# Optimization experiments

Hardware: AMD Instinct MI355X
Metric: run time of the kernel (lower is better)

The kernel has to match this reference:

```python
import jax, jax.numpy as jnp
import numpy as np

B, N, K = 8, 2048, 100  # graphs per batch, nodes per graph, diffpool clusters


def _bn(x, g, b, eps=1e-5):
    # BatchNorm1d in training mode over all B*N nodes (biased variance)
    m = x.mean(axis=(0, 1))
    v = x.var(axis=(0, 1))
    return (x - m) * jax.lax.rsqrt(v + eps) * g + b


def _norm_adj(A):
    # PyG gcn_norm: add remaining self-loops (fill=1), D^-1/2 (A+I) D^-1/2
    n = A.shape[-1]
    d = jnp.diagonal(A, axis1=-2, axis2=-1)
    A_hat = A + jnp.where(d == 0, 1.0, 0.0)[..., :, None] * jnp.eye(n, dtype=A.dtype)
    deg = A_hat.sum(-1)
    dinv = jnp.where(deg > 0, 1.0 / jnp.sqrt(deg), 0.0)
    return dinv[..., :, None] * A_hat * dinv[..., None, :]


def _gcn(An, x, W, b):
    # GCNConv: propagate(x @ W) + bias, with pre-normalized adjacency
    return An @ (x @ W) + b


def _forward(x, adj, W_in, W3030, Wp13, b30, b100, Wfc_pool, bfc_pool,
             W1, b1, W2, b2, gamma30, beta30, gamma100, beta100):
    A_w = _norm_adj(adj)                               # weighted (edge_attr) adjacency
    A_b = _norm_adj((adj > 0).astype(adj.dtype))       # pool convs ignore edge_attr
    # feature branch
    x11 = _bn(_gcn(A_w, x, W_in[0], b30[0]), gamma30[0], beta30[0])
    x12 = _bn(_gcn(A_w, x11, W3030[0], b30[1]), gamma30[1], beta30[1])
    x13 = _bn(_gcn(A_w, x12, W3030[1], b30[2]), gamma30[2], beta30[2])
    x1_out = jnp.concatenate([x11, x12, x13], -1).max(axis=1)   # [B,90]
    # assignment branch
    s11 = _bn(_gcn(A_b, x, W_in[1], b30[3]), gamma30[3], beta30[3])
    s12 = _bn(_gcn(A_b, s11, W3030[2], b30[4]), gamma30[4], beta30[4])
    s13 = _bn(_gcn(A_b, s12, Wp13, b100), gamma100, beta100)
    s1 = jnp.concatenate([s11, s12, s13], -1) @ Wfc_pool + bfc_pool  # [B,N,K]
    # dense_diff_pool (link/entropy losses are unused by the forward output)
    s = jax.nn.softmax(s1, -1)
    p1_x = jnp.einsum('bnk,bnd->bkd', s, x13)          # s^T x  [B,K,30]
    p1_adj = jnp.einsum('bnk,bnl->bkl', s, adj @ s)    # s^T A s  [B,K,K]
    # second stage on pooled (dense, weighted) graph
    A2 = _norm_adj(p1_adj)
    x21 = _bn(_gcn(A2, p1_x, W3030[3], b30[5]), gamma30[5], beta30[5])
    x22 = _bn(_gcn(A2, x21, W3030[4], b30[6]), gamma30[6], beta30[6])
    x23 = _bn(_gcn(A2, x22, W3030[5], b30[7]), gamma30[7], beta30[7])
    x2_out = jnp.concatenate([x21, x22, x23], -1).max(axis=1)   # [B,90]
    h = jnp.concatenate([x1_out, x2_out], -1) @ W1 + b1
    return jax.nn.relu(h) @ W2 + b2                    # [B,6]


def setup_inputs():
    key = jax.random.key(0)
    ks = jax.random.split(key, 12)
    u = jax.random.uniform(ks[0], (B, N, N), dtype=jnp.float32)
    mask = jax.random.uniform(ks[1], (B, N, N)) < 0.05
    A = jnp.triu(u * mask, 1)
    adj = A + jnp.swapaxes(A, -1, -2)
    x = jax.random.normal(ks[2], (B, N, 3), dtype=jnp.float32)
    w = lambda k, s: jax.random.normal(k, s, dtype=jnp.float32) * 0.1
    return dict(
        x=x, adj=adj,
        W_in=w(ks[3], (2, 3, 30)),      # conv11, pool_conv11
        W3030=w(ks[4], (6, 30, 30)),    # conv12, conv13, pool_conv12, conv21..23
        Wp13=w(ks[5], (30, 100)),
        b30=jnp.zeros((8, 30), jnp.float32),
        b100=jnp.zeros((100,), jnp.float32),
        Wfc_pool=w(ks[6], (160, 100)), bfc_pool=jnp.zeros((100,), jnp.float32),
        W1=w(ks[7], (180, 50)), b1=jnp.zeros((50,), jnp.float32),
        W2=w(ks[8], (50, 6)), b2=jnp.zeros((6,), jnp.float32),
        gamma30=jnp.ones((8, 30), jnp.float32), beta30=jnp.zeros((8, 30), jnp.float32),
        gamma100=jnp.ones((100,), jnp.float32), beta100=jnp.zeros((100,), jnp.float32),
    )


def reference(x, adj, W_in, W3030, Wp13, b30, b100, Wfc_pool, bfc_pool,
              W1, b1, W2, b2, gamma30, beta30, gamma100, beta100):
    return _forward(x, adj, W_in, W3030, Wp13, b30, b100, Wfc_pool, bfc_pool,
                    W1, b1, W2, b2, gamma30, beta30, gamma100, beta100)
```

## Files before the change

kernel.cpp:

```cpp
#include <hip/hip_runtime.h>
#include <hip/hip_fp16.h>
#include <cstdint>
#include <cstddef>

#define BATCH 8
#define NN 2048
#define RTOT 16384
#define CAP 176

static constexpr size_t OF_B1W   = 0;
static constexpr size_t OF_B1B   = 3840;
static constexpr size_t OF_B2W   = 7680;
static constexpr size_t OF_B2B   = 11520;
static constexpr size_t OF_B3W   = 15360;
static constexpr size_t OF_B3B   = 15840;
static constexpr size_t OF_S2    = 17440;
static constexpr size_t OF_CNT   = 17620;
static constexpr size_t ZEND     = 17632;
static constexpr size_t OF_ELLV  = 17664;
static constexpr size_t OF_ELLC  = OF_ELLV + 2883584;
static constexpr size_t OF_ROWLEN= OF_ELLC + 1441792;
static constexpr size_t OF_DINVW = OF_ROWLEN + 16384;
static constexpr size_t OF_DINVB = OF_DINVW + 16384;
static constexpr size_t OF_HWB   = OF_DINVB + 16384;
static constexpr size_t OF_HW3   = OF_HWB + 524288;
static constexpr size_t OF_HB100 = OF_HW3 + 262144;
static constexpr size_t OF_ZW    = OF_HB100 + 851968;
static constexpr size_t OF_ZB    = OF_ZW + 524288;
static constexpr size_t OF_X11   = OF_ZB + 1703936;
static constexpr size_t OF_X12   = OF_X11 + 524288;
static constexpr size_t OF_X13   = OF_X12 + 524288;
static constexpr size_t OF_S11   = OF_X13 + 524288;
static constexpr size_t OF_S12   = OF_S11 + 524288;
static constexpr size_t OF_PARTMAX = OF_S12 + 524288;
static constexpr size_t OF_PP    = OF_PARTMAX + 23040;
static constexpr size_t OF_PPOOL = OF_PP + 3328000;

#define FMA4(acc, s, h) { acc.x += (s)*(h).x; acc.y += (s)*(h).y; acc.z += (s)*(h).z; acc.w += (s)*(h).w; }

__device__ __forceinline__ unsigned short f2h(float f) {
  _Float16 h = (_Float16)f;
  return *(unsigned short*)&h;
}
__device__ __forceinline__ float h2f(unsigned short s) {
  _Float16 h = *(_Float16*)&s;
  return (float)h;
}
__device__ __forceinline__ float2 h2f2(unsigned int u) {
  __half2 h = *(__half2*)&u;
  return __half22float2(h);
}

struct __align__(8) us4 { unsigned short x, y, z, w; };

#define ACC8(g, wt) { \
  float2 f0=h2f2((g).x), f1=h2f2((g).y), f2=h2f2((g).z), f3=h2f2((g).w); \
  acc[0] += (wt)*f0.x; acc[1] += (wt)*f0.y; acc[2] += (wt)*f1.x; acc[3] += (wt)*f1.y; \
  acc[4] += (wt)*f2.x; acc[5] += (wt)*f2.y; acc[6] += (wt)*f3.x; acc[7] += (wt)*f3.y; }


__global__ __launch_bounds__(256) void k_build_ell(
    const float* __restrict__ adj, const float* __restrict__ x,
    const float* __restrict__ Win, float* __restrict__ ellv,
    unsigned short* __restrict__ ellc, int* __restrict__ rowlen,
    float* __restrict__ dinvw, float* __restrict__ dinvb,
    unsigned short* __restrict__ Hwb, float* __restrict__ zbase)
{
  int r = blockIdx.x;
  int t = threadIdx.x, lane = t & 63, wv = t >> 6;
  if (blockIdx.x < 69) {
    int zi = blockIdx.x * 256 + t;
    if (zi < (int)ZEND) zbase[zi] = 0.f;
  }
  const float* row = adj + (size_t)r * NN;
  __shared__ int wcnt[4];
  __shared__ float wsumA[4];
  __shared__ float dsh[2];
  float4 a = ((const float4*)row)[t];
  float4 b = ((const float4*)row)[256 + t];
  float vals[8] = {a.x, a.y, a.z, a.w, b.x, b.y, b.z, b.w};
  int cbase0 = t*4, cbase1 = 1024 + t*4;
  int cnt = 0; float sum = 0.f;
#pragma unroll
  for (int k = 0; k < 8; ++k) { sum += vals[k]; cnt += (vals[k] != 0.f) ? 1 : 0; }
  int pre = cnt;
#pragma unroll
  for (int o = 1; o < 64; o <<= 1) { int n = __shfl_up(pre, o); if (lane >= o) pre += n; }
  int excl = pre - cnt;
  int wtot = __shfl(pre, 63);
#pragma unroll
  for (int o = 32; o; o >>= 1) sum += __shfl_down(sum, o);
  if (lane == 0) { wcnt[wv] = wtot; wsumA[wv] = sum; }
  __syncthreads();
  int base = 0;
  for (int w = 0; w < wv; ++w) base += wcnt[w];
  int p = base + excl;
  size_t rb = (size_t)r * CAP;
#pragma unroll
  for (int k = 0; k < 8; ++k) {
    float v = vals[k];
    if (v != 0.f && p < CAP) {
      ellv[rb + p] = v;
      ellc[rb + p] = (unsigned short)((k < 4) ? (cbase0 + k) : (cbase1 + (k - 4)));
      ++p;
    }
  }
  if (t == 0) {
    int tot = wcnt[0] + wcnt[1] + wcnt[2] + wcnt[3];
    float ws = wsumA[0] + wsumA[1] + wsumA[2] + wsumA[3];
    int nnz = tot < CAP ? tot : CAP;
    int n = nnz;
    while ((n & 3) && n < CAP) { ellv[rb + n] = 0.f; ellc[rb + n] = 0; ++n; }
    rowlen[r] = n;
    float dw = rsqrtf(ws + 1.f), db = rsqrtf((float)nnz + 1.f);
    dinvw[r] = dw; dinvb[r] = db;
    dsh[0] = dw; dsh[1] = db;
  }
  __syncthreads();
  if (t < 64) {
    int c = t & 31, side = t >> 5;
    float v = 0.f;
    if (c < 30) {
      float x0 = x[r*3], x1 = x[r*3+1], x2 = x[r*3+2];
      const float* W = Win + side*90;
      v = (x0*W[c] + x1*W[30+c] + x2*W[60+c]) * dsh[side];
    }
    Hwb[(size_t)r*64 + t] = f2h(v);
  }
}

__global__ __launch_bounds__(256) void k_spmm_pair(
    const unsigned short* __restrict__ Hwb, const float* __restrict__ ellv,
    const unsigned short* __restrict__ ellc, const int* __restrict__ rowlen,
    const float* __restrict__ dinvw, const float* __restrict__ dinvb,
    float* __restrict__ Zw, float* __restrict__ Zb,
    float* __restrict__ bktW, float* __restrict__ bktB)
{
  __shared__ float zsW[32][32];
  __shared__ float zsB[32][32];
  int t = threadIdx.x;
  int gid = blockIdx.x * 256 + t;
  int row = gid >> 3, q = gid & 7;
  int side = q >> 2, sub = q & 3;
  int len = rowlen[row];
  const float4* ev = (const float4*)(ellv + (size_t)row * CAP);
  const uint2*  ec = (const uint2*) (ellc + (size_t)row * CAP);
  const uint4* HP = (const uint4*)(Hwb + (size_t)(row >> 11) * (NN*64));
  float acc[8] = {0,0,0,0,0,0,0,0};
  int nit = len >> 2;
  int i = 0;
  for (; i + 2 <= nit; i += 2) {
    float4 v0 = ev[i], v1 = ev[i+1];
    uint2 cc0 = ec[i], cc1 = ec[i+1];
    int a0 = cc0.x & 0xffff, a1 = cc0.x >> 16, a2 = cc0.y & 0xffff, a3 = cc0.y >> 16;
    int e0 = cc1.x & 0xffff, e1 = cc1.x >> 16, e2 = cc1.y & 0xffff, e3 = cc1.y >> 16;
    uint4 g0 = HP[a0*8+q], g1 = HP[a1*8+q], g2 = HP[a2*8+q], g3 = HP[a3*8+q];
    uint4 g4 = HP[e0*8+q], g5 = HP[e1*8+q], g6 = HP[e2*8+q], g7 = HP[e3*8+q];
    float w0 = side ? (v0.x>0.f?1.f:0.f) : v0.x;
    float w1 = side ? (v0.y>0.f?1.f:0.f) : v0.y;
    float w2 = side ? (v0.z>0.f?1.f:0.f) : v0.z;
    float w3 = side ? (v0.w>0.f?1.f:0.f) : v0.w;
    float w4 = side ? (v1.x>0.f?1.f:0.f) : v1.x;
    float w5 = side ? (v1.y>0.f?1.f:0.f) : v1.y;
    float w6 = side ? (v1.z>0.f?1.f:0.f) : v1.z;
    float w7 = side ? (v1.w>0.f?1.f:0.f) : v1.w;
    ACC8(g0, w0); ACC8(g1, w1); ACC8(g2, w2); ACC8(g3, w3);
    ACC8(g4, w4); ACC8(g5, w5); ACC8(g6, w6); ACC8(g7, w7);
  }
  if (i < nit) {
    float4 v = ev[i];
    uint2 cc = ec[i];
    int c0 = cc.x & 0xffff, c1 = cc.x >> 16, c2 = cc.y & 0xffff, c3 = cc.y >> 16;
    uint4 g0 = HP[c0*8+q], g1 = HP[c1*8+q], g2 = HP[c2*8+q], g3 = HP[c3*8+q];
    float w0 = side ? (v.x>0.f?1.f:0.f) : v.x;
    float w1 = side ? (v.y>0.f?1.f:0.f) : v.y;
    float w2 = side ? (v.z>0.f?1.f:0.f) : v.z;
    float w3 = side ? (v.w>0.f?1.f:0.f) : v.w;
    ACC8(g0, w0); ACC8(g1, w1); ACC8(g2, w2); ACC8(g3, w3);
  }
  uint4 hs = HP[(row & (NN-1))*8 + q];
  ACC8(hs, 1.f);
  float d = side ? dinvb[row] : dinvw[row];
#pragma unroll
  for (int k = 0; k < 8; ++k) acc[k] *= d;
  float* Zp = (side ? Zb : Zw) + (size_t)row*32 + sub*8;
  float4 o0 = {acc[0],acc[1],acc[2],acc[3]}, o1 = {acc[4],acc[5],acc[6],acc[7]};
  ((float4*)Zp)[0] = o0; ((float4*)Zp)[1] = o1;
  int rowloc = t >> 3;
  float (*zs)[32] = side ? zsB : zsW;
#pragma unroll
  for (int k = 0; k < 8; ++k) zs[rowloc][sub*8+k] = acc[k];
  __syncthreads();
  int copy = blockIdx.x & 63;
  if (t < 30) {
    float s1 = 0.f, s2 = 0.f;
    for (int r = 0; r < 32; ++r) { float v = zsW[r][t]; s1 += v; s2 += v*v; }
    atomicAdd(&bktW[(t*64+copy)*2],   s1);
    atomicAdd(&bktW[(t*64+copy)*2+1], s2);
  } else if (t >= 64 && t < 94) {
    int c = t - 64;
    float s1 = 0.f, s2 = 0.f;
    for (int r = 0; r < 32; ++r) { float v = zsB[r][c]; s1 += v; s2 += v*v; }
    atomicAdd(&bktB[(c*64+copy)*2],   s1);
    atomicAdd(&bktB[(c*64+copy)*2+1], s2);
  }
}

__global__ __launch_bounds__(256) void k_spmm_l3(
    const unsigned short* __restrict__ Hw3, const unsigned short* __restrict__ Hb100,
    const float* __restrict__ ellv, const unsigned short* __restrict__ ellc,
    const int* __restrict__ rowlen, const float* __restrict__ dinvw,
    const float* __restrict__ dinvb, float* __restrict__ Zw, float* __restrict__ Zb,
    float* __restrict__ bktW3, float* __restrict__ bktB3)
{
  __shared__ float zs[64][32];
  __shared__ float st[200];
  int t = threadIdx.x;
  if (blockIdx.x < 256) {
    int gid = blockIdx.x * 256 + t;
    int row = gid >> 2, q = gid & 3;
    int len = rowlen[row];
    const float4* ev = (const float4*)(ellv + (size_t)row * CAP);
    const uint2*  ec = (const uint2*) (ellc + (size_t)row * CAP);
    const uint4* HP = (const uint4*)(Hw3 + (size_t)(row >> 11) * (NN*32));
    float acc[8] = {0,0,0,0,0,0,0,0};
    int nit = len >> 2;
    int i = 0;
    for (; i + 2 <= nit; i += 2) {
      float4 v0 = ev[i], v1 = ev[i+1];
      uint2 cc0 = ec[i], cc1 = ec[i+1];
      int a0 = cc0.x & 0xffff, a1 = cc0.x >> 16, a2 = cc0.y & 0xffff, a3 = cc0.y >> 16;
      int e0 = cc1.x & 0xffff, e1 = cc1.x >> 16, e2 = cc1.y & 0xffff, e3 = cc1.y >> 16;
      uint4 g0 = HP[a0*4+q], g1 = HP[a1*4+q], g2 = HP[a2*4+q], g3 = HP[a3*4+q];
      uint4 g4 = HP[e0*4+q], g5 = HP[e1*4+q], g6 = HP[e2*4+q], g7 = HP[e3*4+q];
      ACC8(g0, v0.x); ACC8(g1, v0.y); ACC8(g2, v0.z); ACC8(g3, v0.w);
      ACC8(g4, v1.x); ACC8(g5, v1.y); ACC8(g6, v1.z); ACC8(g7, v1.w);
    }
    if (i < nit) {
      float4 v = ev[i];
      uint2 cc = ec[i];
      int c0 = cc.x & 0xffff, c1 = cc.x >> 16, c2 = cc.y & 0xffff, c3 = cc.y >> 16;
      uint4 g0 = HP[c0*4+q], g1 = HP[c1*4+q], g2 = HP[c2*4+q], g3 = HP[c3*4+q];
      ACC8(g0, v.x); ACC8(g1, v.y); ACC8(g2, v.z); ACC8(g3, v.w);
    }
    uint4 hs = HP[(row & (NN-1))*4 + q];
    ACC8(hs, 1.f);
    float d = dinvw[row];
#pragma unroll
    for (int k = 0; k < 8; ++k) acc[k] *= d;
    float* Zp = Zw + (size_t)row*32 + q*8;
    float4 o0 = {acc[0],acc[1],acc[2],acc[3]}, o1 = {acc[4],acc[5],acc[6],acc[7]};
    ((float4*)Zp)[0] = o0; ((float4*)Zp)[1] = o1;
    int rowloc = t >> 2;
#pragma unroll
    for (int k = 0; k < 8; ++k) zs[rowloc][q*8+k] = acc[k];
    __syncthreads();
    if (t < 30) {
      float s1 = 0.f, s2 = 0.f;
      for (int r = 0; r < 64; ++r) { float v = zs[r][t]; s1 += v; s2 += v*v; }
      int copy = blockIdx.x & 7;
      atomicAdd(&bktW3[(t*8+copy)*2],   s1);
      atomicAdd(&bktW3[(t*8+copy)*2+1], s2);
    }
  } else {
    int bid = blockIdx.x - 256;
    for (int i = t; i < 200; i += 256) st[i] = 0.f;
    __syncthreads();
    int gid = bid * 256 + t;
    int row = gid / 13, q = gid - row*13;
    int len = rowlen[row];
    const float4* ev = (const float4*)(ellv + (size_t)row * CAP);
    const uint2*  ec = (const uint2*) (ellc + (size_t)row * CAP);
    const uint4* HP = (const uint4*)(Hb100 + (size_t)(row >> 11) * ((size_t)NN*104));
    float acc[8] = {0,0,0,0,0,0,0,0};
    int nit = len >> 2;
    int i = 0;
    for (; i + 2 <= nit; i += 2) {
      float4 v0 = ev[i], v1 = ev[i+1];
      uint2 cc0 = ec[i], cc1 = ec[i+1];
      int a0 = cc0.x & 0xffff, a1 = cc0.x >> 16, a2 = cc0.y & 0xffff, a3 = cc0.y >> 16;
      int e0 = cc1.x & 0xffff, e1 = cc1.x >> 16, e2 = cc1.y & 0xffff, e3 = cc1.y >> 16;
      uint4 g0 = HP[a0*13+q], g1 = HP[a1*13+q], g2 = HP[a2*13+q], g3 = HP[a3*13+q];
      uint4 g4 = HP[e0*13+q], g5 = HP[e1*13+q], g6 = HP[e2*13+q], g7 = HP[e3*13+q];
      float w0 = (v0.x>0.f?1.f:0.f), w1 = (v0.y>0.f?1.f:0.f);
      float w2 = (v0.z>0.f?1.f:0.f), w3 = (v0.w>0.f?1.f:0.f);
      float w4 = (v1.x>0.f?1.f:0.f), w5 = (v1.y>0.f?1.f:0.f);
      float w6 = (v1.z>0.f?1.f:0.f), w7 = (v1.w>0.f?1.f:0.f);
      ACC8(g0, w0); ACC8(g1, w1); ACC8(g2, w2); ACC8(g3, w3);
      ACC8(g4, w4); ACC8(g5, w5); ACC8(g6, w6); ACC8(g7, w7);
    }
    if (i < nit) {
      float4 v = ev[i];
      uint2 cc = ec[i];
      int c0 = cc.x & 0xffff, c1 = cc.x >> 16, c2 = cc.y & 0xffff, c3 = cc.y >> 16;
      uint4 g0 = HP[c0*13+q], g1 = HP[c1*13+q], g2 = HP[c2*13+q], g3 = HP[c3*13+q];
      float w0 = (v.x>0.f?1.f:0.f), w1 = (v.y>0.f?1.f:0.f);
      float w2 = (v.z>0.f?1.f:0.f), w3 = (v.w>0.f?1.f:0.f);
      ACC8(g0, w0); ACC8(g1, w1); ACC8(g2, w2); ACC8(g3, w3);
    }
    uint4 hs = HP[(row & (NN-1))*13 + q];
    ACC8(hs, 1.f);
    float d = dinvb[row];
#pragma unroll
    for (int k = 0; k < 8; ++k) acc[k] *= d;
    float* Zp = Zb + (size_t)row*104 + q*8;
    float4 o0 = {acc[0],acc[1],acc[2],acc[3]}, o1 = {acc[4],acc[5],acc[6],acc[7]};
    ((float4*)Zp)[0] = o0; ((float4*)Zp)[1] = o1;
    int c0 = q*8;
#pragma unroll
    for (int k = 0; k < 8; ++k) {
      int ch = c0 + k;
      if (ch < 100) { atomicAdd(&st[ch*2], acc[k]); atomicAdd(&st[ch*2+1], acc[k]*acc[k]); }
    }
    __syncthreads();
    int copy = bid & 7;
    for (int i2 = t; i2 < 200; i2 += 256)
      atomicAdd(&bktB3[((i2>>1)*8 + copy)*2 + (i2&1)], st[i2]);
  }
}

template<int LEVEL>
__global__ __launch_bounds__(256) void k_apply_gemm(
    const float* __restrict__ Zw, const float* __restrict__ bktW,
    const float* __restrict__ gW, const float* __restrict__ beW,
    float* __restrict__ xst, const float* __restrict__ Ww,
    const float* __restrict__ dinvw,
    const float* __restrict__ Zb, const float* __restrict__ bktB,
    const float* __restrict__ gB, const float* __restrict__ beB,
    float* __restrict__ sst, const float* __restrict__ Wb,
    const float* __restrict__ dinvb,
    unsigned short* __restrict__ HwOut, unsigned short* __restrict__ HbOut)
{
  constexpr int NGB = (LEVEL == 1) ? 8 : 26;
  constexpr int OSTRIDEB = (LEVEL == 1) ? 32 : 104;
  constexpr int NG = 8 + NGB;
  __shared__ float WwL[30*32];
  __shared__ float WbL[30*OSTRIDEB];
  __shared__ float awL[60], abL[60];
  int t = threadIdx.x;
  if (t < 60) {
    int c = t % 30;
    bool isW = t < 30;
    const float4* p = (const float4*)((isW ? bktW : bktB) + c*128);
    float s1 = 0.f, s2 = 0.f;
#pragma unroll
    for (int k = 0; k < 32; ++k) { float4 v = p[k]; s1 += v.x + v.z; s2 += v.y + v.w; }
    float mean = s1/16384.f, var = s2/16384.f - mean*mean, inv = rsqrtf(var + 1e-5f);
    float aa = (isW ? gW : gB)[c]*inv;
    float* dst = isW ? awL : abL;
    dst[c] = aa; dst[30+c] = (isW ? beW : beB)[c] - mean*aa;
  }
  for (int idx = t; idx < 30*32; idx += 256) {
    int k = idx >> 5, c = idx & 31;
    WwL[idx] = (c < 30) ? Ww[k*30 + c] : 0.f;
  }
  if (LEVEL == 1) {
    for (int idx = t; idx < 30*32; idx += 256) {
      int k = idx >> 5, c = idx & 31;
      WbL[idx] = (c < 30) ? Wb[k*30 + c] : 0.f;
    }
  } else {
    for (int idx = t; idx < 30*OSTRIDEB; idx += 256) {
      int k = idx / OSTRIDEB, j = idx % OSTRIDEB;
      WbL[idx] = (j < 100) ? Wb[k*100 + j] : 0.f;
    }
  }
  __syncthreads();
  int gid = blockIdx.x * 256 + t;
  int row = gid / NG, g = gid % NG;
  if (g < 8) {
    const float4* Z4 = (const float4*)Zw + (size_t)row*8;
    float4 z4[8];
#pragma unroll
    for (int u = 0; u < 8; ++u) z4[u] = Z4[u];
    const float* z = (const float*)z4;
    int ch = 4*g;
    float4 zg = Z4[g];
    float4 xv;
    xv.x = (ch+0 < 30) ? awL[ch+0]*zg.x + awL[30+ch+0] : 0.f;
    xv.y = (ch+1 < 30) ? awL[ch+1]*zg.y + awL[30+ch+1] : 0.f;
    xv.z = (ch+2 < 30) ? awL[ch+2]*zg.z + awL[30+ch+2] : 0.f;
    xv.w = (ch+3 < 30) ? awL[ch+3]*zg.w + awL[30+ch+3] : 0.f;
    ((float4*)xst)[(size_t)row*8+g] = xv;
    float4 o = {0,0,0,0};
#pragma unroll
    for (int k = 0; k < 30; ++k) {
      float xk = awL[k]*z[k] + awL[30+k];
      float4 w = *(const float4*)(WwL + k*32 + 4*g);
      FMA4(o, xk, w);
    }
    float d = dinvw[row];
    us4 pv = { f2h(d*o.x), f2h(d*o.y), f2h(d*o.z), f2h(d*o.w) };
    unsigned short* dst = (LEVEL == 1) ? (HwOut + (size_t)row*64 + 4*g)
                                       : (HwOut + (size_t)row*32 + 4*g);
    *(us4*)dst = pv;
  } else {
    int gb = g - 8;
    const float4* Z4 = (const float4*)Zb + (size_t)row*8;
    float4 z4[8];
#pragma unroll
// ... 47 lines not shown
    float mean = s1/16384.f, var = s2/16384.f - mean*mean, inv = rsqrtf(var + 1e-5f);
    float aa = gW3[t]*inv; aw3[t] = aa; aw3[30+t] = beW3[t] - mean*aa;
  } else if (t >= 64 && t < 164) {
    int c = t - 64;
    const float4* p = (const float4*)(bktB3 + c*16);
    float s1 = 0.f, s2 = 0.f;
#pragma unroll
    for (int k = 0; k < 4; ++k) { float4 v = p[k]; s1 += v.x + v.z; s2 += v.y + v.w; }
    float mean = s1/16384.f, var = s2/16384.f - mean*mean, inv = rsqrtf(var + 1e-5f);
    float aa = g100[c]*inv; ab3[c] = aa; ab3[100+c] = be100[c] - mean*aa;
  }
  __syncthreads();
  for (int idx = t; idx < 64*160; idx += 256) {
    int l = idx / 160, c = idx % 160;
    int g = g0 + l;
    float v;
    if (c < 30) v = s11[(size_t)g*32 + c];
    else if (c < 60) v = s12[(size_t)g*32 + (c-30)];
    else { int k = c - 60; v = ab3[k]*Zb3[(size_t)g*104 + k] + ab3[100 + k]; }
    feat[l*160 + c] = v;
  }
  for (int idx = t; idx < 64*32; idx += 256) {
    int l = idx >> 5, c = idx & 31;
    int g = g0 + l;
    x13[(size_t)g*32+c] = (c < 30) ? aw3[c]*Zw3[(size_t)g*32+c] + aw3[30+c] : 0.f;
  }
  int np = t >> 3, kg = t & 7;
  int n0 = np*2, n1 = np*2 + 1;
  int kbase = kg*12 + (kg < 4 ? kg : 4);
  int klen  = kg < 4 ? 13 : 12;
  float a0[13], a1[13];
#pragma unroll
  for (int j = 0; j < 13; ++j) { a0[j] = 0.f; a1[j] = 0.f; }
  for (int ch = 0; ch < 4; ++ch) {
    __syncthreads();
    for (int idx = t; idx < 4000; idx += 256) {
      int r = idx/100, j = idx%100;
      Wl[r*100 + j] = Wfc[(ch*40 + r)*100 + j];
    }
    __syncthreads();
    for (int kk = 0; kk < 40; ++kk) {
      float f0 = feat[n0*160 + ch*40+kk];
      float f1 = feat[n1*160 + ch*40+kk];
#pragma unroll
      for (int j = 0; j < 13; ++j) {
        if (j < klen) {
          float w = Wl[kk*100 + kbase + j];
          a0[j] += f0*w; a1[j] += f1*w;
        }
      }
    }
  }
  __syncthreads();
  float* sRow = shm;
  for (int j = 0; j < klen; ++j) {
    int k = kbase + j;
    sRow[n0*100 + k] = a0[j] + bfc[k];
    sRow[n1*100 + k] = a1[j] + bfc[k];
  }
  __syncthreads();
  int n = t >> 2, part = t & 3;
  int i0 = part*25;
  float m = -3.4e38f;
  for (int i = 0; i < 25; ++i) m = fmaxf(m, sRow[n*100 + i0 + i]);
  m = fmaxf(m, __shfl_xor(m, 1));
  m = fmaxf(m, __shfl_xor(m, 2));
  float ev[25]; float s = 0.f;
  for (int i = 0; i < 25; ++i) { float e = __expf(sRow[n*100 + i0 + i] - m); ev[i] = e; s += e; }
  s += __shfl_xor(s, 1);
  s += __shfl_xor(s, 2);
  float rinv = 1.f / s;
  for (int i = 0; i < 25; ++i) S[(size_t)(g0+n)*104 + i0 + i] = f2h(ev[i] * rinv);
  if (part == 3) {
    S[(size_t)(g0+n)*104 + 100] = 0; S[(size_t)(g0+n)*104 + 101] = 0;
    S[(size_t)(g0+n)*104 + 102] = 0; S[(size_t)(g0+n)*104 + 103] = 0;
  }
}

__global__ __launch_bounds__(256) void k_spmm_as(
    const unsigned short* __restrict__ S, const float* __restrict__ ellv,
    const unsigned short* __restrict__ ellc, const int* __restrict__ rowlen,
    float* __restrict__ Z)
{
  int t = threadIdx.x;
  int gid = blockIdx.x * 256 + t;
  int row = gid / 13, q = gid - row*13;
  int len = rowlen[row];
  const float4* ev = (const float4*)(ellv + (size_t)row * CAP);
  const uint2*  ec = (const uint2*) (ellc + (size_t)row * CAP);
  const uint4* HP = (const uint4*)(S + (size_t)(row >> 11) * ((size_t)NN*104));
  float acc[8] = {0,0,0,0,0,0,0,0};
  int nit = len >> 2;
  int i = 0;
  for (; i + 2 <= nit; i += 2) {
    float4 v0 = ev[i], v1 = ev[i+1];
    uint2 cc0 = ec[i], cc1 = ec[i+1];
    int a0 = cc0.x & 0xffff, a1 = cc0.x >> 16, a2 = cc0.y & 0xffff, a3 = cc0.y >> 16;
    int e0 = cc1.x & 0xffff, e1 = cc1.x >> 16, e2 = cc1.y & 0xffff, e3 = cc1.y >> 16;
    uint4 g0 = HP[a0*13+q], g1 = HP[a1*13+q], g2 = HP[a2*13+q], g3 = HP[a3*13+q];
    uint4 g4 = HP[e0*13+q], g5 = HP[e1*13+q], g6 = HP[e2*13+q], g7 = HP[e3*13+q];
    ACC8(g0, v0.x); ACC8(g1, v0.y); ACC8(g2, v0.z); ACC8(g3, v0.w);
    ACC8(g4, v1.x); ACC8(g5, v1.y); ACC8(g6, v1.z); ACC8(g7, v1.w);
  }
  if (i < nit) {
    float4 v = ev[i];
    uint2 cc = ec[i];
    int c0 = cc.x & 0xffff, c1 = cc.x >> 16, c2 = cc.y & 0xffff, c3 = cc.y >> 16;
    uint4 g0 = HP[c0*13+q], g1 = HP[c1*13+q], g2 = HP[c2*13+q], g3 = HP[c3*13+q];
    ACC8(g0, v.x); ACC8(g1, v.y); ACC8(g2, v.z); ACC8(g3, v.w);
  }
  float* Zp = Z + (size_t)row*104 + q*8;
  float4 o0 = {acc[0],acc[1],acc[2],acc[3]}, o1 = {acc[4],acc[5],acc[6],acc[7]};
  ((float4*)Zp)[0] = o0; ((float4*)Zp)[1] = o1;
}

__global__ __launch_bounds__(256) void k_pool_part(
    const unsigned short* __restrict__ S, const float* __restrict__ x13,
    const float* __restrict__ As, const float* __restrict__ x11,
    const float* __restrict__ x12, float* __restrict__ pp, float* __restrict__ pm)
{
  __shared__ float sL[64][100];
  __shared__ float xL[64][132];
  __shared__ float red[256];
  int t = threadIdx.x;
  int b = blockIdx.x >> 5, chunk = blockIdx.x & 31;
  int g0 = b * 2048 + chunk * 64;
  int kt = t/10, dt = t%10;
  int k0 = kt*4, d0 = dt*13;
  float acc[4][13];
#pragma unroll
  for (int a = 0; a < 4; ++a)
#pragma unroll
    for (int j = 0; j < 13; ++j) acc[a][j] = 0.f;
  for (int idx = t; idx < 64*100; idx += 256) {
    int l = idx/100, k = idx%100;
    sL[l][k] = h2f(S[(size_t)(g0+l)*104 + k]);
  }
  for (int idx = t; idx < 64*130; idx += 256) {
    int l = idx/130, d = idx%130;
    xL[l][d] = d < 30 ? x13[(size_t)(g0+l)*32 + d] : As[(size_t)(g0+l)*104 + (d-30)];
  }
  __syncthreads();
  if (t < 250) {
    for (int kk = 0; kk < 64; ++kk) {
      float sv[4];
#pragma unroll
      for (int a = 0; a < 4; ++a) sv[a] = sL[kk][k0+a];
#pragma unroll
      for (int j = 0; j < 13; ++j) {
        float xv = xL[kk][d0+j];
#pragma unroll
        for (int a = 0; a < 4; ++a) acc[a][j] += sv[a]*xv;
      }
    }
    float* dst = pp + (size_t)blockIdx.x * 13000;
    for (int a = 0; a < 4; ++a)
      for (int j = 0; j < 13; ++j)
        dst[(k0+a)*130 + (d0+j)] = acc[a][j];
  }
  __syncthreads();
  {
    int c = t & 31, rg = t >> 5;
    const float* srcs[3] = {x11, x12, x13};
#pragma unroll
    for (int a = 0; a < 3; ++a) {
      const float* p = srcs[a] + (size_t)(g0+rg)*32 + c;
      float m = -3.4e38f;
#pragma unroll
      for (int it = 0; it < 8; ++it) m = fmaxf(m, p[it*256]);
      red[t] = m;
      __syncthreads();
      if (t < 30) {
        float mm = red[t];
        for (int g = 1; g < 8; ++g) mm = fmaxf(mm, red[g*32+t]);
        pm[(size_t)blockIdx.x*90 + a*30 + t] = mm;
      }
      __syncthreads();
    }
  }
}

__global__ __launch_bounds__(256) void k_pool_reduce(
    const float* __restrict__ pp, float* __restrict__ ppool)
{
  int b = blockIdx.x / 51, blk = blockIdx.x % 51;
  int idx = blk * 256 + threadIdx.x;
  if (idx < 13000) {
    const float* src = pp + (size_t)b * 32 * 13000 + idx;
    float s = 0.f;
#pragma unroll
    for (int c = 0; c < 32; ++c) s += src[c*13000];
    ppool[(size_t)b*13000 + idx] = s;
// ... 102 lines not shown
      atomicAdd(cnt, 1);
      while (atomicAdd(cnt, 0) < (L+1)*8) {}
      __threadfence();
    }
    __syncthreads();
    if (t < 30) {
      float s1 = atomicAdd(&bktS2[(L*30+t)*2],   0.f);
      float s2 = atomicAdd(&bktS2[(L*30+t)*2+1], 0.f);
      float mean = s1/800.f, var = s2/800.f - mean*mean, inv = rsqrtf(var + 1e-5f);
      float aa = g30[L*30+t]*inv;
      coef[t] = aa; coef[30+t] = be30[L*30+t] - mean*aa;
    }
    __syncthreads();
    if (L < 2) {
      for (int idx = t; idx < 3000; idx += 256) {
        int c = idx % 30;
        buf1[idx] = coef[c]*buf1[idx] + coef[30+c];
      }
      __syncthreads();
      if (t < 30) {
        float m = -3.4e38f;
        for (int i = 0; i < 100; ++i) m = fmaxf(m, buf1[i*30+t]);
        x2L[L*30+t] = m;
      }
      __syncthreads();
    } else {
      if (t < 30) {
        float m = -3.4e38f;
        for (int i = 0; i < 100; ++i) m = fmaxf(m, coef[t]*buf1[i*30+t] + coef[30+t]);
        x2L[60+t] = m;
      }
    }
  }
  if (t < 90) {
    float m = -3.4e38f;
    for (int s = 0; s < 32; ++s) m = fmaxf(m, partmax[(size_t)(b*32+s)*90 + t]);
    x1L[t] = m;
  }
  __syncthreads();
  if (t < 50) {
    float a = b1[t];
    for (int k = 0; k < 90; ++k) a += x1L[k]*W1[k*50+t];
    for (int k = 0; k < 90; ++k) a += x2L[k]*W1[(90+k)*50+t];
    hh[t] = fmaxf(a, 0.f);
  }
  __syncthreads();
  if (t < 6) {
    float a = b2[t];
    for (int j = 0; j < 50; ++j) a += hh[j]*W2[j*6+t];
    out[b*6+t] = a;
  }
}

extern "C" void kernel_launch(void* const* d_in, const int* in_sizes, int n_in,
                              void* d_out, int out_size, void* d_ws, size_t ws_size,
                              hipStream_t stream)
{
  const float* x    = (const float*)d_in[0];
  const float* adj  = (const float*)d_in[1];
  const float* Win  = (const float*)d_in[2];
  const float* W3030= (const float*)d_in[3];
  const float* Wp13 = (const float*)d_in[4];
  const float* Wfc  = (const float*)d_in[7];
  const float* bfc  = (const float*)d_in[8];
  const float* W1   = (const float*)d_in[9];
  const float* b1   = (const float*)d_in[10];
  const float* W2   = (const float*)d_in[11];
  const float* b2   = (const float*)d_in[12];
  const float* g30  = (const float*)d_in[13];
  const float* be30 = (const float*)d_in[14];
  const float* g100 = (const float*)d_in[15];
  const float* be100= (const float*)d_in[16];
  float* out = (float*)d_out;

  float* wsf = (float*)d_ws;
  float* bL1W = wsf + OF_B1W;  float* bL1B = wsf + OF_B1B;
  float* bL2W = wsf + OF_B2W;  float* bL2B = wsf + OF_B2B;
  float* bL3W = wsf + OF_B3W;  float* bL3B = wsf + OF_B3B;
  float* bktS2 = wsf + OF_S2;
  int*   cnt  = (int*)(wsf + OF_CNT);
  float* ellv  = wsf + OF_ELLV;
  unsigned short* ellc = (unsigned short*)(wsf + OF_ELLC);
  int*   rowlen = (int*)(wsf + OF_ROWLEN);
  float* dinvw = wsf + OF_DINVW;
  float* dinvb = wsf + OF_DINVB;
  unsigned short* Hwb   = (unsigned short*)(wsf + OF_HWB);
  unsigned short* Hw3   = (unsigned short*)(wsf + OF_HW3);
  unsigned short* Hb100 = (unsigned short*)(wsf + OF_HB100);
  unsigned short* S     = Hb100;
  float* Zw = wsf + OF_ZW;
  float* Zb = wsf + OF_ZB;
  float* x11 = wsf + OF_X11;
  float* x12 = wsf + OF_X12;
  float* x13 = wsf + OF_X13;
  float* s11 = wsf + OF_S11;
  float* s12 = wsf + OF_S12;
  float* pp  = wsf + OF_PP;
  float* ppool = wsf + OF_PPOOL;
  float* partmax = wsf + OF_PARTMAX;

  k_build_ell<<<RTOT, 256, 0, stream>>>(adj, x, Win, ellv, ellc, rowlen, dinvw, dinvb, Hwb, wsf);

  k_spmm_pair<<<512, 256, 0, stream>>>(Hwb, ellv, ellc, rowlen, dinvw, dinvb, Zw, Zb, bL1W, bL1B);
  k_apply_gemm<1><<<1024, 256, 0, stream>>>(Zw, bL1W, g30+0, be30+0, x11, W3030+0, dinvw,
                                            Zb, bL1B, g30+90, be30+90, s11, W3030+2*900, dinvb, Hwb, Hwb);

  k_spmm_pair<<<512, 256, 0, stream>>>(Hwb, ellv, ellc, rowlen, dinvw, dinvb, Zw, Zb, bL2W, bL2B);
  k_apply_gemm<2><<<2176, 256, 0, stream>>>(Zw, bL2W, g30+30, be30+30, x12, W3030+900, dinvw,
                                            Zb, bL2B, g30+120, be30+120, s12, Wp13, dinvb, Hw3, Hb100);

  k_spmm_l3<<<1088, 256, 0, stream>>>(Hw3, Hb100, ellv, ellc, rowlen, dinvw, dinvb, Zw, Zb, bL3W, bL3B);
  k_fcpool<<<256, 256, 0, stream>>>(Zw, bL3W, g30+60, be30+60, Zb, bL3B, g100, be100,
                                    s11, s12, Wfc, bfc, x13, S);

  k_spmm_as<<<832, 256, 0, stream>>>(S, ellv, ellc, rowlen, Zb );
  k_pool_part<<<256, 256, 0, stream>>>(S, x13, Zb, x11, x12, pp, partmax);
  k_pool_reduce<<<408, 256, 0, stream>>>(pp, ppool);

  k_s2fused<<<BATCH, 256, 0, stream>>>(ppool, partmax, W3030+3*900, g30+150, be30+150,
                                       bktS2, cnt, W1, b1, W2, b2, out);
}
```

Baseline: 549.0 us.

## Stage dense feature tiles in LDS for ELL SpMM gathers with sorted columns

The ELL build now emits column indices in ascending order (contiguous 8-element chunks per thread, padding to a multiple of 8) and records the true nnz per row. All SpMM kernels loop over column tiles, cooperatively load each tile of the fp16 feature matrix into shared memory, and gather neighbours from LDS instead of scattered global reads. For the binary-adjacency side, edge weights come from the nnz count, so ellv is not read there. The cost is that every block streams the whole per-graph feature matrix through LDS with many barriers, plus a per-group loop with more branching.

```diff
diff --git a/kernel.cpp b/kernel.cpp
--- a/kernel.cpp
+++ b/kernel.cpp
@@ -20,7 +20,8 @@
 static constexpr size_t OF_ELLV  = 17664;
 static constexpr size_t OF_ELLC  = OF_ELLV + 2883584;
 static constexpr size_t OF_ROWLEN= OF_ELLC + 1441792;
-static constexpr size_t OF_DINVW = OF_ROWLEN + 16384;
+static constexpr size_t OF_NNZ   = OF_ROWLEN + 16384;
+static constexpr size_t OF_DINVW = OF_NNZ + 16384;
 static constexpr size_t OF_DINVB = OF_DINVW + 16384;
 static constexpr size_t OF_HWB   = OF_DINVB + 16384;
 static constexpr size_t OF_HW3   = OF_HWB + 524288;
@@ -63,6 +64,7 @@
     const float* __restrict__ adj, const float* __restrict__ x,
     const float* __restrict__ Win, float* __restrict__ ellv,
     unsigned short* __restrict__ ellc, int* __restrict__ rowlen,
+    int* __restrict__ nnzarr,
     float* __restrict__ dinvw, float* __restrict__ dinvb,
     unsigned short* __restrict__ Hwb, float* __restrict__ zbase)
 {
@@ -76,10 +78,10 @@
   __shared__ int wcnt[4];
   __shared__ float wsumA[4];
   __shared__ float dsh[2];
-  float4 a = ((const float4*)row)[t];
-  float4 b = ((const float4*)row)[256 + t];
+  float4 a = ((const float4*)row)[2*t];
+  float4 b = ((const float4*)row)[2*t + 1];
   float vals[8] = {a.x, a.y, a.z, a.w, b.x, b.y, b.z, b.w};
-  int cbase0 = t*4, cbase1 = 1024 + t*4;
+  int cbase = t*8;
   int cnt = 0; float sum = 0.f;
 #pragma unroll
   for (int k = 0; k < 8; ++k) { sum += vals[k]; cnt += (vals[k] != 0.f) ? 1 : 0; }
@@ -101,7 +103,7 @@
     float v = vals[k];
     if (v != 0.f && p < CAP) {
       ellv[rb + p] = v;
-      ellc[rb + p] = (unsigned short)((k < 4) ? (cbase0 + k) : (cbase1 + (k - 4)));
+      ellc[rb + p] = (unsigned short)(cbase + k);
       ++p;
     }
   }
@@ -110,8 +112,9 @@
     float ws = wsumA[0] + wsumA[1] + wsumA[2] + wsumA[3];
     int nnz = tot < CAP ? tot : CAP;
     int n = nnz;
-    while ((n & 3) && n < CAP) { ellv[rb + n] = 0.f; ellc[rb + n] = 0; ++n; }
+    while ((n & 7) && n < CAP) { ellv[rb + n] = 0.f; ellc[rb + n] = 0; ++n; }
     rowlen[r] = n;
+    nnzarr[r] = nnz;
     float dw = rsqrtf(ws + 1.f), db = rsqrtf((float)nnz + 1.f);
     dinvw[r] = dw; dinvb[r] = db;
     dsh[0] = dw; dsh[1] = db;
@@ -132,54 +135,61 @@
 __global__ __launch_bounds__(256) void k_spmm_pair(
     const unsigned short* __restrict__ Hwb, const float* __restrict__ ellv,
     const unsigned short* __restrict__ ellc, const int* __restrict__ rowlen,
+    const int* __restrict__ nnzarr,
     const float* __restrict__ dinvw, const float* __restrict__ dinvb,
     float* __restrict__ Zw, float* __restrict__ Zb,
     float* __restrict__ bktW, float* __restrict__ bktB)
 {
+  __shared__ uint4 Hl[2048];
   __shared__ float zsW[32][32];
   __shared__ float zsB[32][32];
   int t = threadIdx.x;
-  int gid = blockIdx.x * 256 + t;
-  int row = gid >> 3, q = gid & 7;
-  int side = q >> 2, sub = q & 3;
-  int len = rowlen[row];
+  int row = blockIdx.x * 32 + (t >> 3);
+  int q = t & 7, side = q >> 2, sub = q & 3;
+  int g = row >> 11;
+  int len = rowlen[row], nnz = nnzarr[row];
   const float4* ev = (const float4*)(ellv + (size_t)row * CAP);
   const uint2*  ec = (const uint2*) (ellc + (size_t)row * CAP);
-  const uint4* HP = (const uint4*)(Hwb + (size_t)(row >> 11) * (NN*64));
+  const uint4* HP = (const uint4*)(Hwb + (size_t)g * (NN*64));
   float acc[8] = {0,0,0,0,0,0,0,0};
   int nit = len >> 2;
   int i = 0;
-  for (; i + 2 <= nit; i += 2) {
-    float4 v0 = ev[i], v1 = ev[i+1];
-    uint2 cc0 = ec[i], cc1 = ec[i+1];
-    int a0 = cc0.x & 0xffff, a1 = cc0.x >> 16, a2 = cc0.y & 0xffff, a3 = cc0.y >> 16;
-    int e0 = cc1.x & 0xffff, e1 = cc1.x >> 16, e2 = cc1.y & 0xffff, e3 = cc1.y >> 16;
-    uint4 g0 = HP[a0*8+q], g1 = HP[a1*8+q], g2 = HP[a2*8+q], g3 = HP[a3*8+q];
-    uint4 g4 = HP[e0*8+q], g5 = HP[e1*8+q], g6 = HP[e2*8+q], g7 = HP[e3*8+q];
-    float w0 = side ? (v0.x>0.f?1.f:0.f) : v0.x;
-    float w1 = side ? (v0.y>0.f?1.f:0.f) : v0.y;
-    float w2 = side ? (v0.z>0.f?1.f:0.f) : v0.z;
-    float w3 = side ? (v0.w>0.f?1.f:0.f) : v0.w;
-    float w4 = side ? (v1.x>0.f?1.f:0.f) : v1.x;
-    float w5 = side ? (v1.y>0.f?1.f:0.f) : v1.y;
-    float w6 = side ? (v1.z>0.f?1.f:0.f) : v1.z;
-    float w7 = side ? (v1.w>0.f?1.f:0.f) : v1.w;
-    ACC8(g0, w0); ACC8(g1, w1); ACC8(g2, w2); ACC8(g3, w3);
-    ACC8(g4, w4); ACC8(g5, w5); ACC8(g6, w6); ACC8(g7, w7);
-  }
-  if (i < nit) {
-    float4 v = ev[i];
-    uint2 cc = ec[i];
-    int c0 = cc.x & 0xffff, c1 = cc.x >> 16, c2 = cc.y & 0xffff, c3 = cc.y >> 16;
-    uint4 g0 = HP[c0*8+q], g1 = HP[c1*8+q], g2 = HP[c2*8+q], g3 = HP[c3*8+q];
-    float w0 = side ? (v.x>0.f?1.f:0.f) : v.x;
-    float w1 = side ? (v.y>0.f?1.f:0.f) : v.y;
-    float w2 = side ? (v.z>0.f?1.f:0.f) : v.z;
-    float w3 = side ? (v.w>0.f?1.f:0.f) : v.w;
-    ACC8(g0, w0); ACC8(g1, w1); ACC8(g2, w2); ACC8(g3, w3);
-  }
-  uint4 hs = HP[(row & (NN-1))*8 + q];
-  ACC8(hs, 1.f);
+  for (int tile = 0; tile < 8; ++tile) {
+    int lo = tile << 8, hi = lo + 256;
+    __syncthreads();
+    for (int s = t; s < 2048; s += 256) Hl[s] = HP[(lo << 3) + s];
+    __syncthreads();
+    while (i < nit) {
+      uint2 cc = ec[i];
+      int c0 = cc.x & 0xffff;
+      if (c0 >= hi) break;
+      int c1 = cc.x >> 16, c2 = cc.y & 0xffff, c3 = cc.y >> 16;
+      float w0, w1, w2, w3;
+      if (side) {
+        int ib = i << 2;
+        w0 = (c0 >= lo && ib   < nnz) ? 1.f : 0.f;
+        w1 = (c1 >= lo && c1 < hi && ib+1 < nnz) ? 1.f : 0.f;
+        w2 = (c2 >= lo && c2 < hi && ib+2 < nnz) ? 1.f : 0.f;
+        w3 = (c3 >= lo && c3 < hi && ib+3 < nnz) ? 1.f : 0.f;
+      } else {
+        float4 v = ev[i];
+        w0 = (c0 >= lo) ? v.x : 0.f;
+        w1 = (c1 >= lo && c1 < hi) ? v.y : 0.f;
+        w2 = (c2 >= lo && c2 < hi) ? v.z : 0.f;
+        w3 = (c3 >= lo && c3 < hi) ? v.w : 0.f;
+      }
+      uint4 g0 = Hl[((c0 - lo) & 255)*8 + q];
+      uint4 g1 = Hl[((c1 - lo) & 255)*8 + q];
+      uint4 g2 = Hl[((c2 - lo) & 255)*8 + q];
+      uint4 g3 = Hl[((c3 - lo) & 255)*8 + q];
+      ACC8(g0, w0); ACC8(g1, w1); ACC8(g2, w2); ACC8(g3, w3);
+      if (c1 < hi && c2 < hi && c3 < hi) ++i; else break;
+    }
+  }
+  {
+    uint4 hs = HP[(row & (NN-1))*8 + q];
+    ACC8(hs, 1.f);
+  }
   float d = side ? dinvb[row] : dinvw[row];
 #pragma unroll
   for (int k = 0; k < 8; ++k) acc[k] *= d;
@@ -209,48 +219,58 @@
 __global__ __launch_bounds__(256) void k_spmm_l3(
     const unsigned short* __restrict__ Hw3, const unsigned short* __restrict__ Hb100,
     const float* __restrict__ ellv, const unsigned short* __restrict__ ellc,
-    const int* __restrict__ rowlen, const float* __restrict__ dinvw,
+    const int* __restrict__ rowlen, const int* __restrict__ nnzarr,
+    const float* __restrict__ dinvw,
     const float* __restrict__ dinvb, float* __restrict__ Zw, float* __restrict__ Zb,
     float* __restrict__ bktW3, float* __restrict__ bktB3)
 {
-  __shared__ float zs[64][32];
-  __shared__ float st[200];
+  __shared__ uint4 TL[1664];
+  __shared__ float aux[2048];
   int t = threadIdx.x;
   if (blockIdx.x < 256) {
-    int gid = blockIdx.x * 256 + t;
-    int row = gid >> 2, q = gid & 3;
+    int row = blockIdx.x * 64 + (t >> 2), q = t & 3;
+    int g = row >> 11;
     int len = rowlen[row];
     const float4* ev = (const float4*)(ellv + (size_t)row * CAP);
     const uint2*  ec = (const uint2*) (ellc + (size_t)row * CAP);
-    const uint4* HP = (const uint4*)(Hw3 + (size_t)(row >> 11) * (NN*32));
+    const uint4* HP = (const uint4*)(Hw3 + (size_t)g * (NN*32));
     float acc[8] = {0,0,0,0,0,0,0,0};
     int nit = len >> 2;
     int i = 0;
-    for (; i + 2 <= nit; i += 2) {
-      float4 v0 = ev[i], v1 = ev[i+1];
-      uint2 cc0 = ec[i], cc1 = ec[i+1];
-      int a0 = cc0.x & 0xffff, a1 = cc0.x >> 16, a2 = cc0.y & 0xffff, a3 = cc0.y >> 16;
-      int e0 = cc1.x & 0xffff, e1 = cc1.x >> 16, e2 = cc1.y & 0xffff, e3 = cc1.y >> 16;
-      uint4 g0 = HP[a0*4+q], g1 = HP[a1*4+q], g2 = HP[a2*4+q], g3 = HP[a3*4+q];
-      uint4 g4 = HP[e0*4+q], g5 = HP[e1*4+q], g6 = HP[e2*4+q], g7 = HP[e3*4+q];
-      ACC8(g0, v0.x); ACC8(g1, v0.y); ACC8(g2, v0.z); ACC8(g3, v0.w);
-      ACC8(g4, v1.x); ACC8(g5, v1.y); ACC8(g6, v1.z); ACC8(g7, v1.w);
-    }
-    if (i < nit) {
-      float4 v = ev[i];
-      uint2 cc = ec[i];
-      int c0 = cc.x & 0xffff, c1 = cc.x >> 16, c2 = cc.y & 0xffff, c3 = cc.y >> 16;
-      uint4 g0 = HP[c0*4+q], g1 = HP[c1*4+q], g2 = HP[c2*4+q], g3 = HP[c3*4+q];
-      ACC8(g0, v.x); ACC8(g1, v.y); ACC8(g2, v.z); ACC8(g3, v.w);
-    }
-    uint4 hs = HP[(row & (NN-1))*4 + q];
-    ACC8(hs, 1.f);
+    for (int tile = 0; tile < 8; ++tile) {
+      int lo = tile << 8, hi = lo + 256;
+      __syncthreads();
+      for (int s = t; s < 1024; s += 256) TL[s] = HP[(lo << 2) + s];
+      __syncthreads();
+      while (i < nit) {
+        uint2 cc = ec[i];
+        int c0 = cc.x & 0xffff;
+        if (c0 >= hi) break;
+        int c1 = cc.x >> 16, c2 = cc.y & 0xffff, c3 = cc.y >> 16;
+        float4 v = ev[i];
+        float w0 = (c0 >= lo) ? v.x : 0.f;
+        float w1 = (c1 >= lo && c1 < hi) ? v.y : 0.f;
+        float w2 = (c2 >= lo && c2 < hi) ? v.z : 0.f;
+        float w3 = (c3 >= lo && c3 < hi) ? v.w : 0.f;
+        uint4 g0 = TL[((c0 - lo) & 255)*4 + q];
+        uint4 g1 = TL[((c1 - lo) & 255)*4 + q];
+        uint4 g2 = TL[((c2 - lo) & 255)*4 + q];
+        uint4 g3 = TL[((c3 - lo) & 255)*4 + q];
+        ACC8(g0, w0); ACC8(g1, w1); ACC8(g2, w2); ACC8(g3, w3);
+        if (c1 < hi && c2 < hi && c3 < hi) ++i; else break;
+      }
+    }
+    {
+      uint4 hs = HP[(row & (NN-1))*4 + q];
+      ACC8(hs, 1.f);
+    }
     float d = dinvw[row];
 #pragma unroll
     for (int k = 0; k < 8; ++k) acc[k] *= d;
     float* Zp = Zw + (size_t)row*32 + q*8;
     float4 o0 = {acc[0],acc[1],acc[2],acc[3]}, o1 = {acc[4],acc[5],acc[6],acc[7]};
     ((float4*)Zp)[0] = o0; ((float4*)Zp)[1] = o1;
+    float (*zs)[32] = (float (*)[32])aux;
     int rowloc = t >> 2;
 #pragma unroll
     for (int k = 0; k < 8; ++k) zs[rowloc][q*8+k] = acc[k];
@@ -264,58 +284,59 @@
     }
   } else {
     int bid = blockIdx.x - 256;
-    for (int i = t; i < 200; i += 256) st[i] = 0.f;
-    __syncthreads();
+    for (int s = t; s < 200; s += 256) aux[s] = 0.f;
     int gid = bid * 256 + t;
     int row = gid / 13, q = gid - row*13;
-    int len = rowlen[row];
-    const float4* ev = (const float4*)(ellv + (size_t)row * CAP);
-    const uint2*  ec = (const uint2*) (ellc + (size_t)row * CAP);
-    const uint4* HP = (const uint4*)(Hb100 + (size_t)(row >> 11) * ((size_t)NN*104));
+    int g = row >> 11;
+    int len = rowlen[row], nnz = nnzarr[row];
+    const uint2* ec = (const uint2*)(ellc + (size_t)row * CAP);
+    const uint4* HP = (const uint4*)(Hb100 + (size_t)g * ((size_t)NN*104));
     float acc[8] = {0,0,0,0,0,0,0,0};
     int nit = len >> 2;
     int i = 0;
-    for (; i + 2 <= nit; i += 2) {
-      float4 v0 = ev[i], v1 = ev[i+1];
-      uint2 cc0 = ec[i], cc1 = ec[i+1];
-      int a0 = cc0.x & 0xffff, a1 = cc0.x >> 16, a2 = cc0.y & 0xffff, a3 = cc0.y >> 16;
-      int e0 = cc1.x & 0xffff, e1 = cc1.x >> 16, e2 = cc1.y & 0xffff, e3 = cc1.y >> 16;
-      uint4 g0 = HP[a0*13+q], g1 = HP[a1*13+q], g2 = HP[a2*13+q], g3 = HP[a3*13+q];
-      uint4 g4 = HP[e0*13+q], g5 = HP[e1*13+q], g6 = HP[e2*13+q], g7 = HP[e3*13+q];
-      float w0 = (v0.x>0.f?1.f:0.f), w1 = (v0.y>0.f?1.f:0.f);
-      float w2 = (v0.z>0.f?1.f:0.f), w3 = (v0.w>0.f?1.f:0.f);
-      float w4 = (v1.x>0.f?1.f:0.f), w5 = (v1.y>0.f?1.f:0.f);
-      float w6 = (v1.z>0.f?1.f:0.f), w7 = (v1.w>0.f?1.f:0.f);
-      ACC8(g0, w0); ACC8(g1, w1); ACC8(g2, w2); ACC8(g3, w3);
-      ACC8(g4, w4); ACC8(g5, w5); ACC8(g6, w6); ACC8(g7, w7);
-    }
-    if (i < nit) {
-      float4 v = ev[i];
-      uint2 cc = ec[i];
-      int c0 = cc.x & 0xffff, c1 = cc.x >> 16, c2 = cc.y & 0xffff, c3 = cc.y >> 16;
-      uint4 g0 = HP[c0*13+q], g1 = HP[c1*13+q], g2 = HP[c2*13+q], g3 = HP[c3*13+q];
-      float w0 = (v.x>0.f?1.f:0.f), w1 = (v.y>0.f?1.f:0.f);
-      float w2 = (v.z>0.f?1.f:0.f), w3 = (v.w>0.f?1.f:0.f);
-      ACC8(g0, w0); ACC8(g1, w1); ACC8(g2, w2); ACC8(g3, w3);
-    }
-    uint4 hs = HP[(row & (NN-1))*13 + q];
-    ACC8(hs, 1.f);
+    for (int tile = 0; tile < 16; ++tile) {
+      int lo = tile << 7, hi = lo + 128;
+      __syncthreads();
+      for (int s = t; s < 1664; s += 256) TL[s] = HP[lo*13 + s];
+      __syncthreads();
+      while (i < nit) {
+        uint2 cc = ec[i];
+        int c0 = cc.x & 0xffff;
+        if (c0 >= hi) break;
+        int c1 = cc.x >> 16, c2 = cc.y & 0xffff, c3 = cc.y >> 16;
+        int ib = i << 2;
+        float w0 = (c0 >= lo && ib   < nnz) ? 1.f : 0.f;
+        float w1 = (c1 >= lo && c1 < hi && ib+1 < nnz) ? 1.f : 0.f;
+        float w2 = (c2 >= lo && c2 < hi && ib+2 < nnz) ? 1.f : 0.f;
+        float w3 = (c3 >= lo && c3 < hi && ib+3 < nnz) ? 1.f : 0.f;
+        uint4 g0 = TL[((c0 - lo) & 127)*13 + q];
+        uint4 g1 = TL[((c1 - lo) & 127)*13 + q];
+        uint4 g2 = TL[((c2 - lo) & 127)*13 + q];
+        uint4 g3 = TL[((c3 - lo) & 127)*13 + q];
+        ACC8(g0, w0); ACC8(g1, w1); ACC8(g2, w2); ACC8(g3, w3);
+        if (c1 < hi && c2 < hi && c3 < hi) ++i; else break;
+      }
+    }
+    {
+      uint4 hs = HP[(row & (NN-1))*13 + q];
+      ACC8(hs, 1.f);
+    }
     float d = dinvb[row];
 #pragma unroll
     for (int k = 0; k < 8; ++k) acc[k] *= d;
     float* Zp = Zb + (size_t)row*104 + q*8;
     float4 o0 = {acc[0],acc[1],acc[2],acc[3]}, o1 = {acc[4],acc[5],acc[6],acc[7]};
     ((float4*)Zp)[0] = o0; ((float4*)Zp)[1] = o1;
-    int c0 = q*8;
+    int c0b = q*8;
 #pragma unroll
     for (int k = 0; k < 8; ++k) {
-      int ch = c0 + k;
-      if (ch < 100) { atomicAdd(&st[ch*2], acc[k]); atomicAdd(&st[ch*2+1], acc[k]*acc[k]); }
+      int ch = c0b + k;
+      if (ch < 100) { atomicAdd(&aux[ch*2], acc[k]); atomicAdd(&aux[ch*2+1], acc[k]*acc[k]); }
     }
     __syncthreads();
     int copy = bid & 7;
     for (int i2 = t; i2 < 200; i2 += 256)
-      atomicAdd(&bktB3[((i2>>1)*8 + copy)*2 + (i2&1)], st[i2]);
+      atomicAdd(&bktB3[((i2>>1)*8 + copy)*2 + (i2&1)], aux[i2]);
   }
 }
 
@@ -529,32 +550,40 @@
     const unsigned short* __restrict__ ellc, const int* __restrict__ rowlen,
     float* __restrict__ Z)
 {
+  __shared__ uint4 TL[1664];
   int t = threadIdx.x;
   int gid = blockIdx.x * 256 + t;
   int row = gid / 13, q = gid - row*13;
+  int g = row >> 11;
   int len = rowlen[row];
   const float4* ev = (const float4*)(ellv + (size_t)row * CAP);
   const uint2*  ec = (const uint2*) (ellc + (size_t)row * CAP);
-  const uint4* HP = (const uint4*)(S + (size_t)(row >> 11) * ((size_t)NN*104));
+  const uint4* HP = (const uint4*)(S + (size_t)g * ((size_t)NN*104));
   float acc[8] = {0,0,0,0,0,0,0,0};
   int nit = len >> 2;
   int i = 0;
-  for (; i + 2 <= nit; i += 2) {
-    float4 v0 = ev[i], v1 = ev[i+1];
-    uint2 cc0 = ec[i], cc1 = ec[i+1];
-    int a0 = cc0.x & 0xffff, a1 = cc0.x >> 16, a2 = cc0.y & 0xffff, a3 = cc0.y >> 16;
-    int e0 = cc1.x & 0xffff, e1 = cc1.x >> 16, e2 = cc1.y & 0xffff, e3 = cc1.y >> 16;
-    uint4 g0 = HP[a0*13+q], g1 = HP[a1*13+q], g2 = HP[a2*13+q], g3 = HP[a3*13+q];
-    uint4 g4 = HP[e0*13+q], g5 = HP[e1*13+q], g6 = HP[e2*13+q], g7 = HP[e3*13+q];
-    ACC8(g0, v0.x); ACC8(g1, v0.y); ACC8(g2, v0.z); ACC8(g3, v0.w);
-    ACC8(g4, v1.x); ACC8(g5, v1.y); ACC8(g6, v1.z); ACC8(g7, v1.w);
-  }
-  if (i < nit) {
-    float4 v = ev[i];
-    uint2 cc = ec[i];
-    int c0 = cc.x & 0xffff, c1 = cc.x >> 16, c2 = cc.y & 0xffff, c3 = cc.y >> 16;
-    uint4 g0 = HP[c0*13+q], g1 = HP[c1*13+q], g2 = HP[c2*13+q], g3 = HP[c3*13+q];
-    ACC8(g0, v.x); ACC8(g1, v.y); ACC8(g2, v.z); ACC8(g3, v.w);
+  for (int tile = 0; tile < 16; ++tile) {
+    int lo = tile << 7, hi = lo + 128;
+    __syncthreads();
+    for (int s = t; s < 1664; s += 256) TL[s] = HP[lo*13 + s];
+    __syncthreads();
+    while (i < nit) {
+      uint2 cc = ec[i];
+      int c0 = cc.x & 0xffff;
+      if (c0 >= hi) break;
+      int c1 = cc.x >> 16, c2 = cc.y & 0xffff, c3 = cc.y >> 16;
+      float4 v = ev[i];
+      float w0 = (c0 >= lo) ? v.x : 0.f;
+      float w1 = (c1 >= lo && c1 < hi) ? v.y : 0.f;
+      float w2 = (c2 >= lo && c2 < hi) ? v.z : 0.f;
+      float w3 = (c3 >= lo && c3 < hi) ? v.w : 0.f;
+      uint4 g0 = TL[((c0 - lo) & 127)*13 + q];
+      uint4 g1 = TL[((c1 - lo) & 127)*13 + q];
+      uint4 g2 = TL[((c2 - lo) & 127)*13 + q];
+      uint4 g3 = TL[((c3 - lo) & 127)*13 + q];
+      ACC8(g0, w0); ACC8(g1, w1); ACC8(g2, w2); ACC8(g3, w3);
+      if (c1 < hi && c2 < hi && c3 < hi) ++i; else break;
+    }
   }
   float* Zp = Z + (size_t)row*104 + q*8;
   float4 o0 = {acc[0],acc[1],acc[2],acc[3]}, o1 = {acc[4],acc[5],acc[6],acc[7]};
@@ -823,6 +852,7 @@
   float* ellv  = wsf + OF_ELLV;
   unsigned short* ellc = (unsigned short*)(wsf + OF_ELLC);
   int*   rowlen = (int*)(wsf + OF_ROWLEN);
+  int*   nnzarr = (int*)(wsf + OF_NNZ);
   float* dinvw = wsf + OF_DINVW;
   float* dinvb = wsf + OF_DINVB;
   unsigned short* Hwb   = (unsigned short*)(wsf + OF_HWB);
@@ -840,17 +870,21 @@
   float* ppool = wsf + OF_PPOOL;
   float* partmax = wsf + OF_PARTMAX;
 
-  k_build_ell<<<RTOT, 256, 0, stream>>>(adj, x, Win, ellv, ellc, rowlen, dinvw, dinvb, Hwb, wsf);
-
-  k_spmm_pair<<<512, 256, 0, stream>>>(Hwb, ellv, ellc, rowlen, dinvw, dinvb, Zw, Zb, bL1W, bL1B);
+  k_build_ell<<<RTOT, 256, 0, stream>>>(adj, x, Win, ellv, ellc, rowlen, nnzarr,
+                                        dinvw, dinvb, Hwb, wsf);
+
+  k_spmm_pair<<<512, 256, 0, stream>>>(Hwb, ellv, ellc, rowlen, nnzarr, dinvw, dinvb,
+                                       Zw, Zb, bL1W, bL1B);
   k_apply_gemm<1><<<1024, 256, 0, stream>>>(Zw, bL1W, g30+0, be30+0, x11, W3030+0, dinvw,
                                             Zb, bL1B, g30+90, be30+90, s11, W3030+2*900, dinvb, Hwb, Hwb);
 
-  k_spmm_pair<<<512, 256, 0, stream>>>(Hwb, ellv, ellc, rowlen, dinvw, dinvb, Zw, Zb, bL2W, bL2B);
+  k_spmm_pair<<<512, 256, 0, stream>>>(Hwb, ellv, ellc, rowlen, nnzarr, dinvw, dinvb,
+                                       Zw, Zb, bL2W, bL2B);
   k_apply_gemm<2><<<2176, 256, 0, stream>>>(Zw, bL2W, g30+30, be30+30, x12, W3030+900, dinvw,
                                             Zb, bL2B, g30+120, be30+120, s12, Wp13, dinvb, Hw3, Hb100);
 
-  k_spmm_l3<<<1088, 256, 0, stream>>>(Hw3, Hb100, ellv, ellc, rowlen, dinvw, dinvb, Zw, Zb, bL3W, bL3B);
+  k_spmm_l3<<<1088, 256, 0, stream>>>(Hw3, Hb100, ellv, ellc, rowlen, nnzarr, dinvw, dinvb,
+                                      Zw, Zb, bL3W, bL3B);
   k_fcpool<<<256, 256, 0, stream>>>(Zw, bL3W, g30+60, be30+60, Zb, bL3B, g100, be100,
                                     s11, s12, Wfc, bfc, x13, S);
 
```

Measured after the change: 716.5 us. 1.31x slower.
